# Optimization experiments

Measured on AMD Instinct MI355X. Metric: run time of the kernel, lower is better.

Reference implementation:

```python
import jax, jax.numpy as jnp
import numpy as np

K = 3       # kernel_size
STRIDE = 1
PAD = 1


def conv2d(x, w, b):
    y = jax.lax.conv_general_dilated(
        x, w, window_strides=(STRIDE, STRIDE), padding=[(PAD, PAD), (PAD, PAD)],
        dimension_numbers=('NCHW', 'OIHW', 'NCHW'))
    return y + b[None, :, None, None]


def setup_inputs() -> dict:
    key = jax.random.key(0)
    ks = jax.random.split(key, 4)
    B, Cin, Cout, H, W = 8, 64, 64, 64, 64
    kk = K * K
    x = jax.random.normal(ks[0], (B, Cin, H, W), jnp.float32)
    # offset / modulator convs (zero-init in the original; use small random weights
    # so offsets are nontrivial but realistic sub-pixel scale)
    w_off = jax.random.normal(ks[1], (2 * kk, Cin, K, K), jnp.float32) * 0.01
    b_off = jnp.zeros((2 * kk,), jnp.float32)
    w_mod = jax.random.normal(ks[2], (kk, Cin, K, K), jnp.float32) * 0.01
    b_mod = jnp.zeros((kk,), jnp.float32)
    # main deformable conv weight, Kaiming-ish scale
    w = jax.random.normal(ks[3], (Cout, Cin, K, K), jnp.float32) * (1.0 / np.sqrt(Cin * kk))
    b = jnp.zeros((Cout,), jnp.float32)
    return {"x": x, "w_off": w_off, "b_off": b_off,
            "w_mod": w_mod, "b_mod": b_mod, "w": w, "b": b}


def deform_conv2d(x, offset, mask, w, b):
    # torchvision deform_conv2d semantics, deformable_groups=1, groups=1.
    B, C, H, W = x.shape
    kk = K * K
    Ho = (H + 2 * PAD - K) // STRIDE + 1
    Wo = (W + 2 * PAD - K) // STRIDE + 1
    # offset channels are interleaved (dy, dx) pairs per kernel tap
    off = offset.reshape(B, kk, 2, Ho, Wo)
    kh, kw = jnp.meshgrid(jnp.arange(K), jnp.arange(K), indexing='ij')
    kh = kh.reshape(kk).astype(x.dtype)
    kw = kw.reshape(kk).astype(x.dtype)
    base_y = (jnp.arange(Ho) * STRIDE - PAD).astype(x.dtype)
    base_x = (jnp.arange(Wo) * STRIDE - PAD).astype(x.dtype)
    # sampling coordinates in input space: [B, kk, Ho, Wo]
    ys = base_y[None, None, :, None] + kh[None, :, None, None] + off[:, :, 0]
    xs = base_x[None, None, None, :] + kw[None, :, None, None] + off[:, :, 1]
    y0 = jnp.floor(ys)
    x0 = jnp.floor(xs)

    def gather(yi, xi):
        yc = jnp.clip(yi, 0, H - 1).astype(jnp.int32)
        xc = jnp.clip(xi, 0, W - 1).astype(jnp.int32)
        # per-batch fancy gather: [C, H, W] indexed by [kk, Ho, Wo] -> [C, kk, Ho, Wo]
        return jax.vmap(lambda img, yb, xb: img[:, yb, xb])(x, yc, xc)

    acc = jnp.zeros((B, C, kk, Ho, Wo), x.dtype)
    for dy, dx in ((0, 0), (0, 1), (1, 0), (1, 1)):
        yi = y0 + dy
        xi = x0 + dx
        wgt = (1.0 - jnp.abs(ys - yi)) * (1.0 - jnp.abs(xs - xi))
        # zero-padding semantics: corners outside the input contribute 0
        valid = (yi >= 0) & (yi <= H - 1) & (xi >= 0) & (xi <= W - 1)
        wgt = jnp.where(valid, wgt, 0.0)
        acc = acc + gather(yi, xi) * wgt[:, None]
    # modulate with sigmoid mask [B, kk, Ho, Wo], then contract with conv weight
    sampled = acc * mask[:, None]
    out = jnp.einsum('bcfij,ocf->boij', sampled, w.reshape(w.shape[0], C, kk))
    return out + b[None, :, None, None]


def reference(x, w_off, b_off, w_mod, b_mod, w, b):
    offset = conv2d(x, w_off, b_off)
    mask = jax.nn.sigmoid(conv2d(x, w_mod, b_mod))
    return deform_conv2d(x, offset, mask, w, b)
```

## Files before the change

### kernel.cpp

```cpp
#include <hip/hip_runtime.h>
#include <math.h>

#define HW    64
#define NPIX  32768

typedef __attribute__((ext_vector_type(8))) short bf16x8;
typedef __attribute__((ext_vector_type(8))) short short8v;
typedef __attribute__((ext_vector_type(4))) float f32x4;

static __device__ inline short f2bf(float f) {
    union { float f; unsigned u; } v; v.f = f;
    unsigned r = v.u + 0x7fff + ((v.u >> 16) & 1);
    return (short)(r >> 16);
}

__global__ __launch_bounds__(256) void k_misc(
        const float* __restrict__ x, short* __restrict__ xt,
        const float* __restrict__ w, const float* __restrict__ w_off,
        const float* __restrict__ w_mod,
        short* __restrict__ wt3, short* __restrict__ wc2) {
    int tid = threadIdx.x;
    if (blockIdx.x < 512) {
        __shared__ float s[64 * 65];
        int by = blockIdx.x;
        int b = by >> 6, y = by & 63;
        const float* xb = x + ((size_t)b * 64) * 4096 + y * 64;
        #pragma unroll
        for (int q = 0; q < 4; ++q) {
            int fi = q * 256 + tid;
            int c = fi >> 4, xq = (fi & 15) * 4;
            float4 v = *(const float4*)(xb + (size_t)c * 4096 + xq);
            s[c * 65 + xq + 0] = v.x; s[c * 65 + xq + 1] = v.y;
            s[c * 65 + xq + 2] = v.z; s[c * 65 + xq + 3] = v.w;
        }
        __syncthreads();
        short* dst = xt + ((size_t)(b * 64 + y)) * 4096;
        #pragma unroll
        for (int q = 0; q < 4; ++q) {
            int fi = q * 256 + tid;
            int xx = fi >> 4, c = (fi & 15) * 4;
            short4 v = make_short4(f2bf(s[(c + 0) * 65 + xx]), f2bf(s[(c + 1) * 65 + xx]),
                                   f2bf(s[(c + 2) * 65 + xx]), f2bf(s[(c + 3) * 65 + xx]));
            *(short4*)(dst + xx * 64 + c) = v;
        }
    } else {
        int t = (blockIdx.x - 512) * 256 + tid;
        if (t < 36864) {
            int wv = t / 9216, r = t - wv * 9216;
            int f  = r >> 10;
            int r2 = r & 1023;
            int kk = r2 >> 9, lane = (r2 >> 3) & 63, j = r2 & 7;
            int o = wv * 16 + (lane & 15);
            int c = kk * 32 + (lane >> 4) * 8 + j;
            wt3[t] = f2bf(w[(o * 64 + c) * 9 + f]);
        }
        int u = t - 36864;
        if (u >= 0 && u < 9 * 32 * 64) {
            int c = u & 63, ch = (u >> 6) & 31, f = u >> 11;
            float v = 0.f;
            if (ch < 18)      v = w_off[(ch * 64 + c) * 9 + f];
            else if (ch < 27) v = w_mod[((ch - 18) * 64 + c) * 9 + f];
            wc2[u] = f2bf(v);
        }
    }
}

__global__ __launch_bounds__(256) void k_convmetaG(
        const short* __restrict__ xt,
        const short* __restrict__ wc2, const short* __restrict__ wt3,
        const float* __restrict__ b_off, const float* __restrict__ b_mod,
        float4* __restrict__ metaW, int4* __restrict__ metaO,
        short* __restrict__ G) {
    __shared__ __align__(16) char smem[18432];
    float* s_out = (float*)(smem + 13824);

    int tid  = threadIdx.x;
    int lane = tid & 63;
    int wv   = __builtin_amdgcn_readfirstlane((int)(tid >> 6));
    int blk  = blockIdx.x;
    int b = blk >> 7, i = (blk >> 1) & 63, jb = (blk & 1) * 32;
    int P0 = blk * 32;
    const short* xs = xt + (size_t)b * 262144;
    int arow = lane & 15, cg = lane >> 4, cgb = cg * 8;

    for (int u = tid; u < 864; u += 256) {
        int cell = u >> 3, chunk = u & 7;
        int r = cell / 36, cc = cell - r * 36;
        int y = i - 1 + r, gx = jb + cc - 2;
        short8v v = (short8v){0,0,0,0,0,0,0,0};
        if (((unsigned)y < 64u) & ((unsigned)gx < 64u))
            v = *(const short8v*)(xs + ((y << 6) + gx) * 64 + chunk * 8);
        *(short8v*)(smem + cell * 128 + ((chunk * 16) ^ ((cell & 7) << 4))) = v;
    }
    __syncthreads();

    {
        int mh = wv & 1, nh = wv >> 1;
        f32x4 acc = (f32x4){0.f, 0.f, 0.f, 0.f};
        #pragma unroll
        for (int ky = 0; ky < 3; ++ky)
            #pragma unroll
            for (int kx = 0; kx < 3; ++kx) {
                int f = ky * 3 + kx;
                #pragma unroll
                for (int kk = 0; kk < 2; ++kk) {
                    bf16x8 bq = *(const bf16x8*)(wc2 + (f * 32 + nh * 16 + arow) * 64
                                                 + kk * 32 + cgb);
                    int cell = ky * 36 + mh * 16 + arow + kx + 1;
                    const char* ap = smem + cell * 128
                                   + ((kk * 64 + cg * 16) ^ ((cell & 7) << 4));
                    acc = __builtin_amdgcn_mfma_f32_16x16x32_bf16(
                        *(const bf16x8*)ap, bq, acc, 0, 0, 0);
                }
            }
        #pragma unroll
        for (int r = 0; r < 4; ++r)
            s_out[(nh * 16 + arow) * 36 + mh * 16 + cg * 4 + r] = acc[r];
    }
    __syncthreads();

    for (int u = tid; u < 288; u += 256) {
        int f = u >> 5, p = u & 31;
        float dy = s_out[(2 * f)     * 36 + p] + b_off[2 * f];
        float dx = s_out[(2 * f + 1) * 36 + p] + b_off[2 * f + 1];
        float mv = s_out[(18 + f)    * 36 + p] + b_mod[f];
        float m  = 1.f / (1.f + expf(-mv));

        float ys  = (float)(i - 1 + f / 3) + dy;
        float xs2 = (float)(jb + p - 1 + f % 3) + dx;
        float y0f = floorf(ys), x0f = floorf(xs2);
        int   y0  = (int)y0f,   x0  = (int)x0f;
        float fy = ys - y0f, fx = xs2 - x0f;

        bool vy0 = (unsigned)y0       < 64u, vy1 = (unsigned)(y0 + 1) < 64u;
        bool vx0 = (unsigned)x0       < 64u, vx1 = (unsigned)(x0 + 1) < 64u;
        float w00 = (vy0 & vx0) ? (1.f - fy) * (1.f - fx) * m : 0.f;
        float w01 = (vy0 & vx1) ? (1.f - fy) * fx         * m : 0.f;
        float w10 = (vy1 & vx0) ? fy         * (1.f - fx) * m : 0.f;
        float w11 = (vy1 & vx1) ? fy         * fx         * m : 0.f;

        int y0c = min(max(y0, 0), 63), y1c = min(max(y0 + 1, 0), 63);
        int x0c = min(max(x0, 0), 63), x1c = min(max(x0 + 1, 0), 63);

        metaW[f * NPIX + P0 + p] = make_float4(w00, w01, w10, w11);
        metaO[f * NPIX + P0 + p] = make_int4(((y0c << 6) + x0c) * 128,
                                             ((y0c << 6) + x1c) * 128,
                                             ((y1c << 6) + x0c) * 128,
                                             ((y1c << 6) + x1c) * 128);
    }

    bf16x8 wfrag[9][2];
    #pragma unroll
    for (int f = 0; f < 9; ++f)
        #pragma unroll
        for (int kk = 0; kk < 2; ++kk)
            wfrag[f][kk] = *(const bf16x8*)(wt3 + ((wv * 18 + f * 2 + kk) * 64 + lane) * 8);

    #pragma unroll
    for (int f = 0; f < 9; ++f) {
        f32x4 g[2];
        g[0] = (f32x4){0.f, 0.f, 0.f, 0.f};
        g[1] = (f32x4){0.f, 0.f, 0.f, 0.f};
        #pragma unroll
        for (int kk = 0; kk < 2; ++kk)
            #pragma unroll
            for (int nf = 0; nf < 2; ++nf) {
                int cell = 36 + nf * 16 + arow + 2;
                const char* bp = smem + cell * 128
                               + ((kk * 64 + cg * 16) ^ ((cell & 7) << 4));
                g[nf] = __builtin_amdgcn_mfma_f32_16x16x32_bf16(
                    wfrag[f][kk], *(const bf16x8*)bp, g[nf], 0, 0, 0);
            }
        #pragma unroll
        for (int nf = 0; nf < 2; ++nf) {
            unsigned w0, w1;
            asm("v_cvt_pk_bf16_f32 %0, %1, %2" : "=v"(w0) : "v"(g[nf][0]), "v"(g[nf][1]));
            asm("v_cvt_pk_bf16_f32 %0, %1, %2" : "=v"(w1) : "v"(g[nf][2]), "v"(g[nf][3]));
            size_t base = (size_t)(f * NPIX + P0 + nf * 16 + arow) * 64 + wv * 16 + cg * 4;
            *(int2*)(G + base) = make_int2((int)w0, (int)w1);
        }
    }
}

__global__ __launch_bounds__(256, 4) void k_final(
        const short* __restrict__ G,
        const float4* __restrict__ metaW, const int4* __restrict__ metaO,
        const float* __restrict__ bias, float* __restrict__ out) {
    __shared__ float s_o[8][66];
    int tid  = threadIdx.x;
    int lane = tid & 63;
    int wv   = __builtin_amdgcn_readfirstlane((int)(tid >> 6));
    int bid  = blockIdx.x;
    int b = bid & 7, q = bid >> 3;
    int i = q >> 3, j0 = (q & 7) * 8;
    int P0 = b * 4096 + q * 8;
    int cp = lane & 31;
    bool hi = lane >= 32;
    const char* Gb = (const char*)G + (size_t)b * 524288;

    float a00 = 0.f, a01 = 0.f, a10 = 0.f, a11 = 0.f;
    #pragma unroll
    for (int pxi = 0; pxi < 2; ++pxi) {
        int P = P0 + wv * 2 + pxi;
        float accL = 0.f, accH = 0.f;
        #pragma unroll
        for (int f = 0; f < 9; ++f) {
            float4 mW = metaW[f * NPIX + P];
            int4   mO = metaO[f * NPIX + P];
            const char* Gf = Gb + (size_t)f * 4194304;
            unsigned g0 = *(const unsigned*)(Gf + (hi ? mO.y : mO.x) + cp * 4);
            unsigned g1 = *(const unsigned*)(Gf + (hi ? mO.w : mO.z) + cp * 4);
            float wA = hi ? mW.y : mW.x;
            float wB = hi ? mW.w : mW.z;
            union { unsigned u; float f; } l0, h0, l1, h1;
            l0.u = g0 << 16; h0.u = g0 & 0xffff0000u;
            l1.u = g1 << 16; h1.u = g1 & 0xffff0000u;
            accL += wA * l0.f + wB * l1.f;
            accH += wA * h0.f + wB * h1.f;
        }
        if (pxi == 0) { a00 = accL; a01 = accH; }
        else          { a10 = accL; a11 = accH; }
    }
    a00 += __shfl_xor(a00, 32); a01 += __shfl_xor(a01, 32);
    a10 += __shfl_xor(a10, 32); a11 += __shfl_xor(a11, 32);
    if (!hi) {
        s_o[wv * 2 + 0][2 * cp] = a00; s_o[wv * 2 + 0][2 * cp + 1] = a01;
        s_o[wv * 2 + 1][2 * cp] = a10; s_o[wv * 2 + 1][2 * cp + 1] = a11;
    }
    __syncthreads();
    {
        int o = tid >> 2, jq = tid & 3;
        float bv = bias[o];
        float2 v;
        v.x = s_o[jq * 2 + 0][o] + bv;
        v.y = s_o[jq * 2 + 1][o] + bv;
        *(float2*)(out + ((size_t)(b * 64 + o)) * 4096 + i * 64 + j0 + jq * 2) = v;
    }
}

extern "C" void kernel_launch(void* const* d_in, const int* in_sizes, int n_in,
                              void* d_out, int out_size, void* d_ws, size_t ws_size,
                              hipStream_t stream) {
    const float* x     = (const float*)d_in[0];
    const float* w_off = (const float*)d_in[1];
    const float* b_off = (const float*)d_in[2];
    const float* w_mod = (const float*)d_in[3];
    const float* b_mod = (const float*)d_in[4];
    const float* w     = (const float*)d_in[5];
    const float* bias  = (const float*)d_in[6];
    float* out = (float*)d_out;

    char* ws = (char*)d_ws;
    short*  xt    = (short*)(ws);
    short*  wt3   = (short*)(ws + 4194304);
    short*  wc2   = (short*)(ws + 4268032);
    float4* metaW = (float4*)(ws + 4304896);
    int4*   metaO = (int4*)(ws + 9023488);
    short*  G     = (short*)(ws + 13742080);

    hipLaunchKernelGGL(k_misc,      dim3(728),  dim3(256), 0, stream,
                       x, xt, w, w_off, w_mod, wt3, wc2);
    hipLaunchKernelGGL(k_convmetaG, dim3(1024), dim3(256), 0, stream,
                       xt, wc2, wt3, b_off, b_mod, metaW, metaO, G);
    hipLaunchKernelGGL(k_final,     dim3(4096), dim3(256), 0, stream,
                       G, metaW, metaO, bias, out);
}
```

Baseline: 55.28 us.

## Batch-interleave block mapping and widen final gather to four pixels per wave

k_misc and k_convmetaG now interleave batch indices across consecutive block IDs, which likely spreads each batch's data over XCDs/L2 slices so that locality is better for later readers. k_final handles 16 pixels per block (4 per wave) with half the grid. All 9 taps' gather loads are issued before the accumulation, which raises memory-level parallelism, and output stores become float4. This costs more registers per thread and may lower occupancy under the launch bound of 4.

```diff
diff --git a/kernel.cpp b/kernel.cpp
--- a/kernel.cpp
+++ b/kernel.cpp
@@ -22,8 +22,8 @@
     int tid = threadIdx.x;
     if (blockIdx.x < 512) {
         __shared__ float s[64 * 65];
-        int by = blockIdx.x;
-        int b = by >> 6, y = by & 63;
+        int bid = blockIdx.x;
+        int b = bid & 7, y = bid >> 3;
         const float* xb = x + ((size_t)b * 64) * 4096 + y * 64;
         #pragma unroll
         for (int q = 0; q < 4; ++q) {
@@ -77,7 +77,8 @@
     int tid  = threadIdx.x;
     int lane = tid & 63;
     int wv   = __builtin_amdgcn_readfirstlane((int)(tid >> 6));
-    int blk  = blockIdx.x;
+    int bid  = blockIdx.x;
+    int blk  = (bid & 7) * 128 + (bid >> 3);
     int b = blk >> 7, i = (blk >> 1) & 63, jb = (blk & 1) * 32;
     int P0 = blk * 32;
     const short* xs = xt + (size_t)b * 262144;
@@ -186,55 +187,70 @@
         const short* __restrict__ G,
         const float4* __restrict__ metaW, const int4* __restrict__ metaO,
         const float* __restrict__ bias, float* __restrict__ out) {
-    __shared__ float s_o[8][66];
+    __shared__ float s_o[16][66];
     int tid  = threadIdx.x;
     int lane = tid & 63;
     int wv   = __builtin_amdgcn_readfirstlane((int)(tid >> 6));
     int bid  = blockIdx.x;
     int b = bid & 7, q = bid >> 3;
-    int i = q >> 3, j0 = (q & 7) * 8;
-    int P0 = b * 4096 + q * 8;
+    int i = q >> 2, j0 = (q & 3) * 16;
+    int P0 = b * 4096 + q * 16;
     int cp = lane & 31;
     bool hi = lane >= 32;
     const char* Gb = (const char*)G + (size_t)b * 524288;
 
-    float a00 = 0.f, a01 = 0.f, a10 = 0.f, a11 = 0.f;
-    #pragma unroll
-    for (int pxi = 0; pxi < 2; ++pxi) {
-        int P = P0 + wv * 2 + pxi;
-        float accL = 0.f, accH = 0.f;
+    float aL[4], aH[4];
+    #pragma unroll
+    for (int k = 0; k < 4; ++k) { aL[k] = 0.f; aH[k] = 0.f; }
+
+    #pragma unroll
+    for (int pxi = 0; pxi < 4; ++pxi) {
+        int P = P0 + wv * 4 + pxi;
+        unsigned g0a[9], g1a[9];
+        float wAa[9], wBa[9];
         #pragma unroll
         for (int f = 0; f < 9; ++f) {
             float4 mW = metaW[f * NPIX + P];
             int4   mO = metaO[f * NPIX + P];
             const char* Gf = Gb + (size_t)f * 4194304;
-            unsigned g0 = *(const unsigned*)(Gf + (hi ? mO.y : mO.x) + cp * 4);
-            unsigned g1 = *(const unsigned*)(Gf + (hi ? mO.w : mO.z) + cp * 4);
-            float wA = hi ? mW.y : mW.x;
-            float wB = hi ? mW.w : mW.z;
+            g0a[f] = *(const unsigned*)(Gf + (hi ? mO.y : mO.x) + cp * 4);
+            g1a[f] = *(const unsigned*)(Gf + (hi ? mO.w : mO.z) + cp * 4);
+            wAa[f] = hi ? mW.y : mW.x;
+            wBa[f] = hi ? mW.w : mW.z;
+        }
+        float accL = 0.f, accH = 0.f;
+        #pragma unroll
+        for (int f = 0; f < 9; ++f) {
             union { unsigned u; float f; } l0, h0, l1, h1;
-            l0.u = g0 << 16; h0.u = g0 & 0xffff0000u;
-            l1.u = g1 << 16; h1.u = g1 & 0xffff0000u;
-            accL += wA * l0.f + wB * l1.f;
-            accH += wA * h0.f + wB * h1.f;
-        }
-        if (pxi == 0) { a00 = accL; a01 = accH; }
-        else          { a10 = accL; a11 = accH; }
-    }
-    a00 += __shfl_xor(a00, 32); a01 += __shfl_xor(a01, 32);
-    a10 += __shfl_xor(a10, 32); a11 += __shfl_xor(a11, 32);
+            l0.u = g0a[f] << 16; h0.u = g0a[f] & 0xffff0000u;
+            l1.u = g1a[f] << 16; h1.u = g1a[f] & 0xffff0000u;
+            accL += wAa[f] * l0.f + wBa[f] * l1.f;
+            accH += wAa[f] * h0.f + wBa[f] * h1.f;
+        }
+        aL[pxi] = accL; aH[pxi] = accH;
+    }
+    #pragma unroll
+    for (int k = 0; k < 4; ++k) {
+        aL[k] += __shfl_xor(aL[k], 32);
+        aH[k] += __shfl_xor(aH[k], 32);
+    }
     if (!hi) {
-        s_o[wv * 2 + 0][2 * cp] = a00; s_o[wv * 2 + 0][2 * cp + 1] = a01;
-        s_o[wv * 2 + 1][2 * cp] = a10; s_o[wv * 2 + 1][2 * cp + 1] = a11;
+        #pragma unroll
+        for (int k = 0; k < 4; ++k) {
+            s_o[wv * 4 + k][2 * cp]     = aL[k];
+            s_o[wv * 4 + k][2 * cp + 1] = aH[k];
+        }
     }
     __syncthreads();
     {
         int o = tid >> 2, jq = tid & 3;
         float bv = bias[o];
-        float2 v;
-        v.x = s_o[jq * 2 + 0][o] + bv;
-        v.y = s_o[jq * 2 + 1][o] + bv;
-        *(float2*)(out + ((size_t)(b * 64 + o)) * 4096 + i * 64 + j0 + jq * 2) = v;
+        float4 v;
+        v.x = s_o[jq * 4 + 0][o] + bv;
+        v.y = s_o[jq * 4 + 1][o] + bv;
+        v.z = s_o[jq * 4 + 2][o] + bv;
+        v.w = s_o[jq * 4 + 3][o] + bv;
+        *(float4*)(out + ((size_t)(b * 64 + o)) * 4096 + i * 64 + j0 + jq * 4) = v;
     }
 }
 
@@ -262,6 +278,6 @@
                        x, xt, w, w_off, w_mod, wt3, wc2);
     hipLaunchKernelGGL(k_convmetaG, dim3(1024), dim3(256), 0, stream,
                        xt, wc2, wt3, b_off, b_mod, metaW, metaO, G);
-    hipLaunchKernelGGL(k_final,     dim3(4096), dim3(256), 0, stream,
+    hipLaunchKernelGGL(k_final,     dim3(2048), dim3(256), 0, stream,
                        G, metaW, metaO, bias, out);
 }
```

After: 64.15 us. 1.16x slower.
